# Performance work log

Measured on AMD Instinct MI355X. Metric: run time of the kernel, lower is better.

## Reference

```python
import jax, jax.numpy as jnp
import numpy as np

N, E, H, D_IN, D_OUT, DEPTH, G = 100000, 1600000, 128, 128, 10, 3, 256


def setup_inputs() -> dict:
    key = jax.random.key(0)
    ks = jax.random.split(key, 16)
    s = lambda k, shape: jax.random.normal(k, shape, dtype=jnp.float32) * 0.05
    inp = {
        "x": jax.random.normal(ks[0], (N, D_IN), dtype=jnp.float32),
        "edge_index": jax.random.randint(ks[1], (2, E), 0, N, dtype=jnp.int32),
        "control_edge_index": jax.random.randint(ks[2], (2, 1024), 0, N, dtype=jnp.int32),
        "batch": jnp.sort(jax.random.randint(ks[3], (N,), 0, G, dtype=jnp.int32)),
        # encoder MLP: input_dim -> hidden -> hidden
        "enc_w1": s(ks[4], (D_IN, H)), "enc_b1": jnp.zeros((H,), jnp.float32),
        "enc_w2": s(ks[5], (H, H)),    "enc_b2": jnp.zeros((H,), jnp.float32),
        # conv_depth GCN layers, hidden -> hidden
        "conv_w": s(ks[6], (DEPTH, H, H)), "conv_b": jnp.zeros((DEPTH, H), jnp.float32),
        # decoder MLP: hidden -> hidden -> output_dim
        "dec_w1": s(ks[7], (H, H)),     "dec_b1": jnp.zeros((H,), jnp.float32),
        "dec_w2": s(ks[8], (H, D_OUT)), "dec_b2": jnp.zeros((D_OUT,), jnp.float32),
    }
    return inp


def _gcn_forward(x, enc_w1, enc_b1, enc_w2, enc_b2, conv_w, conv_b,
                 dec_w1, dec_b1, dec_w2, dec_b2, edge_index, batch):
    # encoder MLP (Linear-ReLU-Dropout(eval)-Linear)
    h = jax.nn.relu(x @ enc_w1 + enc_b1) @ enc_w2 + enc_b2

    # GCN normalization with self-loops: D^{-1/2} (A + I) D^{-1/2}
    loops = jnp.arange(N, dtype=edge_index.dtype)
    src = jnp.concatenate([edge_index[0], loops])  # [E + N]
    dst = jnp.concatenate([edge_index[1], loops])
    deg = jax.ops.segment_sum(jnp.ones_like(src, dtype=h.dtype), dst, num_segments=N)
    inv_sqrt = jax.lax.rsqrt(deg)  # deg >= 1 thanks to self-loops
    coef = (inv_sqrt[src] * inv_sqrt[dst])[:, None]  # [E+N, 1]

    for l in range(DEPTH):
        hw = h @ conv_w[l] + conv_b[l]                      # [N, H]
        h = jax.ops.segment_sum(hw[src] * coef, dst, num_segments=N)
        if l < DEPTH - 1:  # linear=False -> nonlinearity between convs
            h = jax.nn.relu(h)

    # global_add_pool over graph ids
    pooled = jax.ops.segment_sum(h, batch, num_segments=G)   # [G, H]

    # decoder MLP
    return jax.nn.relu(pooled @ dec_w1 + dec_b1) @ dec_w2 + dec_b2  # [G, D_OUT]


def reference(x, edge_index, control_edge_index, batch, enc_w1, enc_b1, enc_w2,
              enc_b2, conv_w, conv_b, dec_w1, dec_b1, dec_w2, dec_b2):
    # control_edge_index corresponds to the (disabled) control mechanism; unused
    return _gcn_forward(x, enc_w1, enc_b1, enc_w2, enc_b2, conv_w, conv_b,
                        dec_w1, dec_b1, dec_w2, dec_b2, edge_index, batch)
```

## Files before the change

kernel.cpp:

```cpp
#include <hip/hip_runtime.h>
#include <hip/hip_bf16.h>
#include <cstdint>
#include <cstddef>

#define NN 100000
#define NE 1600000
#define HH 128
#define NG 256

#define NB 196
#define BSH 9
#define BMSK 511
#define CHUNK 16384
#define NBLK 98

typedef __bf16 bf16x8 __attribute__((ext_vector_type(8)));
typedef float floatx4 __attribute__((ext_vector_type(4)));

__device__ __forceinline__ uint32_t f2b(float f) {
  union { float f; uint32_t u; } v; v.f = f;
  uint32_t u = v.u;
  return (u + 0x7FFFu + ((u >> 16) & 1u)) >> 16;
}
__device__ __forceinline__ float blo(uint32_t u) {
  union { uint32_t u; float f; } v; v.u = u << 16;
  return v.f;
}
__device__ __forceinline__ float bhi(uint32_t u) {
  union { uint32_t u; float f; } v; v.u = u & 0xFFFF0000u;
  return v.f;
}
__device__ __forceinline__ void addrow(float* a, uint4 v) {
  a[0] += blo(v.x); a[1] += bhi(v.x);
  a[2] += blo(v.y); a[3] += bhi(v.y);
  a[4] += blo(v.z); a[5] += bhi(v.z);
  a[6] += blo(v.w); a[7] += bhi(v.w);
}

__device__ __forceinline__ void stage_w(uint16_t (*Wt)[136], const float* __restrict__ W,
                                        int tid) {
  for (int it = 0; it < 16; ++it) {
    int idx = tid + it * 256;
    int n = idx & 127;
    int k0 = (idx >> 7) * 4;
    uint2 wv;
    wv.x = f2b(W[(k0 + 0) * 128 + n]) | (f2b(W[(k0 + 1) * 128 + n]) << 16);
    wv.y = f2b(W[(k0 + 2) * 128 + n]) | (f2b(W[(k0 + 3) * 128 + n]) << 16);
    *(uint2*)&Wt[n][k0] = wv;
  }
}


__global__ __launch_bounds__(256) void k_cntA(const int* __restrict__ src,
                                              int* __restrict__ blkcnt) {
  __shared__ int h[NB];
  int t = threadIdx.x;
  if (t < NB) h[t] = 0;
  __syncthreads();
  int base = blockIdx.x * CHUNK, end = min(base + CHUNK, NE);
  for (int i = base + t; i < end; i += 256) atomicAdd(&h[src[i] >> BSH], 1);
  __syncthreads();
  if (t < NB) blkcnt[blockIdx.x * NB + t] = h[t];
}

__global__ __launch_bounds__(256) void k_cntB(const uint2* __restrict__ pairs,
                                              int* __restrict__ blkcnt) {
  __shared__ int h[NB];
  int t = threadIdx.x;
  if (t < NB) h[t] = 0;
  __syncthreads();
  int base = blockIdx.x * CHUNK, end = min(base + CHUNK, NE);
  for (int i = base + t; i < end; i += 256) atomicAdd(&h[pairs[i].y >> BSH], 1);
  __syncthreads();
  if (t < NB) blkcnt[blockIdx.x * NB + t] = h[t];
}

__global__ void k_scan(const int* __restrict__ blkcnt, int* __restrict__ poff,
                       int* __restrict__ gbase, int* __restrict__ off, int set_off) {
  __shared__ int s[256];
  int t = threadIdx.x;
  int tot = 0;
  if (t < NB) {
    for (int r = 0; r < NBLK; ++r) {
      poff[r * NB + t] = tot;
      tot += blkcnt[r * NB + t];
    }
  }
  s[t] = (t < NB) ? tot : 0;
  __syncthreads();
  for (int d = 1; d < 256; d <<= 1) {
    int v = (t >= d) ? s[t - d] : 0;
    __syncthreads();
    s[t] += v;
    __syncthreads();
  }
  if (t < NB) gbase[t] = s[t] - tot;
  if (t == 0) { gbase[NB] = NE; if (set_off) off[NN] = NE; }
}

__global__ __launch_bounds__(256) void k_placeA(const int* __restrict__ src,
                                                const int* __restrict__ dst,
                                                const int* __restrict__ poff,
                                                const int* __restrict__ gbase,
                                                uint2* __restrict__ pairs) {
  __shared__ int cur[NB];
  int t = threadIdx.x;
  if (t < NB) cur[t] = poff[blockIdx.x * NB + t] + gbase[t];
  __syncthreads();
  int base = blockIdx.x * CHUNK, end = min(base + CHUNK, NE);
  for (int i = base + t; i < end; i += 256) {
    int s = src[i], d = dst[i];
    int p = atomicAdd(&cur[s >> BSH], 1);
    pairs[p] = make_uint2((unsigned)s, (unsigned)d);
  }
}

__global__ __launch_bounds__(256) void k_placeB(const uint2* __restrict__ pairs,
                                                const int* __restrict__ poff,
                                                const int* __restrict__ gbase,
                                                uint32_t* __restrict__ outb) {
  __shared__ int cur[NB];
  int t = threadIdx.x;
  if (t < NB) cur[t] = poff[blockIdx.x * NB + t] + gbase[t];
  __syncthreads();
  int base = blockIdx.x * CHUNK, end = min(base + CHUNK, NE);
  for (int i = base + t; i < end; i += 256) {
    uint2 v = pairs[i];
    int p = atomicAdd(&cur[v.y >> BSH], 1);
    outb[p] = v.x | ((v.y & (unsigned)BMSK) << 17);
  }
}

__global__ __launch_bounds__(256) void k_bucket_sort(
    const uint32_t* __restrict__ pairbuf, const int* __restrict__ gbase,
    const int* __restrict__ batch,
    int* __restrict__ off, float* __restrict__ inv, int* __restrict__ csrs,
    int* __restrict__ dhist2, int* __restrict__ gstart)
{
  __shared__ int cnt[512];
  __shared__ int loff[512];
  __shared__ int psum[256];
  int b = blockIdx.x;
  int tid = threadIdx.x;
  cnt[tid] = 0; cnt[tid + 256] = 0;
  __syncthreads();
  int s0 = gbase[b], s1 = gbase[b + 1];
  for (int i = s0 + tid; i < s1; i += 256)
    atomicAdd(&cnt[pairbuf[i] >> 17], 1);
  __syncthreads();
  int a0 = cnt[2 * tid], a1 = cnt[2 * tid + 1];
  int s = a0 + a1;
  psum[tid] = s;
  __syncthreads();
  for (int d = 1; d < 256; d <<= 1) {
    int v = (tid >= d) ? psum[tid - d] : 0;
    __syncthreads();
    psum[tid] += v;
    __syncthreads();
  }
  int excl = psum[tid] - s;
  loff[2 * tid] = excl;
  loff[2 * tid + 1] = excl + a0;
  __syncthreads();
  int* h64 = psum;
  if (tid < 64) h64[tid] = 0;
  __syncthreads();
#pragma unroll
  for (int k = 0; k < 2; ++k) {
    int i = tid + k * 256;
    int node = b * 512 + i;
    if (node < NN) {
      off[node] = s0 + loff[i];
      inv[node] = rsqrtf((float)cnt[i] + 1.0f);
      int d = cnt[i]; if (d > 63) d = 63;
      atomicAdd(&h64[d], 1);
    }
  }
  {
    int n0 = b * 512, n1 = min(n0 + 512, NN);
    for (int i = n0 + tid; i < n1; i += 256) {
      int bb = batch[i];
      if (i == 0) { for (int g = 0; g <= bb; ++g) gstart[g] = 0; }
      else { int aa = batch[i - 1]; for (int g = aa + 1; g <= bb; ++g) gstart[g] = i; }
      if (i == NN - 1) { for (int g = bb + 1; g <= NG; ++g) gstart[g] = NN; }
    }
  }
  __syncthreads();
  if (tid < 64) dhist2[b * 64 + tid] = h64[tid];
  cnt[tid] = loff[tid]; cnt[tid + 256] = loff[tid + 256];
  __syncthreads();
  for (int i = s0 + tid; i < s1; i += 256) {
    uint32_t v = pairbuf[i];
    int p = atomicAdd(&cnt[v >> 17], 1);
    csrs[s0 + p] = (int)(v & 0x1FFFFu);
  }
}

__global__ void k_dscan(const int* __restrict__ dhist2, int* __restrict__ dcur) {
  int t = threadIdx.x;
  int sum = 0;
  for (int r = 0; r < NB; ++r) sum += dhist2[r * 64 + (63 - t)];
  int v = sum;
  for (int d = 1; d < 64; d <<= 1) { int u = __shfl_up(v, d); if (t >= d) v += u; }
  dcur[63 - t] = v - sum;
}

__global__ __launch_bounds__(256) void k_dplace(const int* __restrict__ off,
                                                int* __restrict__ dcur,
                                                int* __restrict__ order) {
  __shared__ int h[64], base[64];
  int t = threadIdx.x;
  if (t < 64) h[t] = 0;
  __syncthreads();
  int i = blockIdx.x * 256 + t;
  int d = 0, ld = 0;
  if (i < NN) { d = off[i + 1] - off[i]; if (d > 63) d = 63; ld = atomicAdd(&h[d], 1); }
  __syncthreads();
  if (t < 64) base[t] = h[t] ? atomicAdd(&dcur[t], h[t]) : 0;
  __syncthreads();
  if (i < NN) order[base[d] + ld] = i;
}

__global__ __launch_bounds__(256) void k_wprep(const float* __restrict__ conv_w,
                                               uint16_t* __restrict__ wbf) {
  int idx = blockIdx.x * 256 + threadIdx.x;
  int l = idx >> 14;
  int n = (idx >> 7) & 127;
  int k = idx & 127;
  wbf[idx] = (uint16_t)f2b(conv_w[(l + 1) * 16384 + k * 128 + n]);
}

__global__ __launch_bounds__(256) void k_gemm(
    const uint16_t* __restrict__ A16, const float* __restrict__ A32,
    const float* __restrict__ W, const float* __restrict__ bias,
    const float* __restrict__ scale,
    uint16_t* __restrict__ Out, int M, int do_relu)
{
  __shared__ uint16_t Wt[128][136];
  const int tid = threadIdx.x;
  stage_w(Wt, W, tid);
  __syncthreads();

  const int lane = tid & 63;
  const int wave = tid >> 6;
  const int lrow = lane & 15;
  const int quad = lane >> 4;
  const int lk = quad * 8;
  const int row0 = blockIdx.x * 128 + wave * 32;

  floatx4 acc[2][8];
#pragma unroll
  for (int t = 0; t < 2; ++t)
#pragma unroll
    for (int n = 0; n < 8; ++n)
      acc[t][n] = (floatx4){0.f, 0.f, 0.f, 0.f};

#pragma unroll
  for (int ks = 0; ks < 4; ++ks) {
    bf16x8 a[2];
#pragma unroll
    for (int t = 0; t < 2; ++t) {
      int r = row0 + t * 16 + lrow;
      uint4 tmp = {0u, 0u, 0u, 0u};
      if (r < M) {
        if (A32) {
          float4 f0 = *(const float4*)(A32 + (size_t)r * HH + ks * 32 + lk);
          float4 f1 = *(const float4*)(A32 + (size_t)r * HH + ks * 32 + lk + 4);
          tmp.x = f2b(f0.x) | (f2b(f0.y) << 16);
          tmp.y = f2b(f0.z) | (f2b(f0.w) << 16);
          tmp.z = f2b(f1.x) | (f2b(f1.y) << 16);
          tmp.w = f2b(f1.z) | (f2b(f1.w) << 16);
        } else {
          tmp = *(const uint4*)(A16 + (size_t)r * HH + ks * 32 + lk);
        }
      }
      a[t] = __builtin_bit_cast(bf16x8, tmp);
    }
#pragma unroll
    for (int n = 0; n < 8; ++n) {
      bf16x8 b = __builtin_bit_cast(bf16x8, *(const uint4*)&Wt[n * 16 + lrow][ks * 32 + lk]);
      acc[0][n] = __builtin_amdgcn_mfma_f32_16x16x32_bf16(b, a[0], acc[0][n], 0, 0, 0);
      acc[1][n] = __builtin_amdgcn_mfma_f32_16x16x32_bf16(b, a[1], acc[1][n], 0, 0, 0);
    }
  }

  float4 b4[8];
#pragma unroll
  for (int n = 0; n < 8; ++n) b4[n] = *(const float4*)(bias + n * 16 + quad * 4);

#pragma unroll
  for (int t = 0; t < 2; ++t) {
    int row = row0 + t * 16 + lrow;
    if (row < M) {
      float sc = scale ? scale[row] : 1.0f;
      uint16_t* orow = Out + (size_t)row * HH;
#pragma unroll
      for (int n = 0; n < 8; ++n) {
        float v0 = acc[t][n][0] + b4[n].x;
        float v1 = acc[t][n][1] + b4[n].y;
        float v2 = acc[t][n][2] + b4[n].z;
        float v3 = acc[t][n][3] + b4[n].w;
        if (do_relu) {
          v0 = fmaxf(v0, 0.f); v1 = fmaxf(v1, 0.f);
          v2 = fmaxf(v2, 0.f); v3 = fmaxf(v3, 0.f);
        }
        v0 *= sc; v1 *= sc; v2 *= sc; v3 *= sc;
        uint2 o;
        o.x = f2b(v0) | (f2b(v1) << 16);
        o.y = f2b(v2) | (f2b(v3) << 16);
        *(uint2*)(orow + n * 16 + quad * 4) = o;
      }
    }
  }
}

__global__ __launch_bounds__(256) void k_gemm_dual(
    const uint16_t* __restrict__ A16,
    const float* __restrict__ Wa, const float* __restrict__ ba,
    const float* __restrict__ Wb, const float* __restrict__ bb,
    const float* __restrict__ scale,
    uint16_t* __restrict__ Out, int M)
{
  __shared__ uint16_t Wt[128][136];
  __shared__ uint16_t tile[128][136];
  const int tid = threadIdx.x;
  stage_w(Wt, Wa, tid);
  __syncthreads();

  const int lane = tid & 63;
  const int wave = tid >> 6;
  const int lrow = lane & 15;
  const int quad = lane >> 4;
  const int lk = quad * 8;
  const int row0 = blockIdx.x * 128 + wave * 32;
  const int trow0 = wave * 32;

  floatx4 acc[2][8];
#pragma unroll
  for (int t = 0; t < 2; ++t)
#pragma unroll
    for (int n = 0; n < 8; ++n)
      acc[t][n] = (floatx4){0.f, 0.f, 0.f, 0.f};

#pragma unroll
  for (int ks = 0; ks < 4; ++ks) {
    bf16x8 a[2];
#pragma unroll
    for (int t = 0; t < 2; ++t) {
      int r = row0 + t * 16 + lrow;
      uint4 tmp = {0u, 0u, 0u, 0u};
      if (r < M) tmp = *(const uint4*)(A16 + (size_t)r * HH + ks * 32 + lk);
      a[t] = __builtin_bit_cast(bf16x8, tmp);
    }
#pragma unroll
    for (int n = 0; n < 8; ++n) {
      bf16x8 b = __builtin_bit_cast(bf16x8, *(const uint4*)&Wt[n * 16 + lrow][ks * 32 + lk]);
      acc[0][n] = __builtin_amdgcn_mfma_f32_16x16x32_bf16(b, a[0], acc[0][n], 0, 0, 0);
      acc[1][n] = __builtin_amdgcn_mfma_f32_16x16x32_bf16(b, a[1], acc[1][n], 0, 0, 0);
    }
  }

  {
    float4 b4[8];
#pragma unroll
    for (int n = 0; n < 8; ++n) b4[n] = *(const float4*)(ba + n * 16 + quad * 4);
#pragma unroll
    for (int t = 0; t < 2; ++t) {
      int trow = trow0 + t * 16 + lrow;
#pragma unroll
      for (int n = 0; n < 8; ++n) {
        uint2 o;
        o.x = f2b(acc[t][n][0] + b4[n].x) | (f2b(acc[t][n][1] + b4[n].y) << 16);
        o.y = f2b(acc[t][n][2] + b4[n].z) | (f2b(acc[t][n][3] + b4[n].w) << 16);
        *(uint2*)&tile[trow][n * 16 + quad * 4] = o;
      }
    }
  }
  __syncthreads();
  stage_w(Wt, Wb, tid);
#pragma unroll
  for (int t = 0; t < 2; ++t)
#pragma unroll
    for (int n = 0; n < 8; ++n)
      acc[t][n] = (floatx4){0.f, 0.f, 0.f, 0.f};
  __syncthreads();

#pragma unroll
  for (int ks = 0; ks < 4; ++ks) {
    bf16x8 a[2];
#pragma unroll
    for (int t = 0; t < 2; ++t)
      a[t] = __builtin_bit_cast(bf16x8,
               *(const uint4*)&tile[trow0 + t * 16 + lrow][ks * 32 + lk]);
#pragma unroll
    for (int n = 0; n < 8; ++n) {
      bf16x8 b = __builtin_bit_cast(bf16x8, *(const uint4*)&Wt[n * 16 + lrow][ks * 32 + lk]);
      acc[0][n] = __builtin_amdgcn_mfma_f32_16x16x32_bf16(b, a[0], acc[0][n], 0, 0, 0);
      acc[1][n] = __builtin_amdgcn_mfma_f32_16x16x32_bf16(b, a[1], acc[1][n], 0, 0, 0);
    }
  }

  {
    float4 b4[8];
#pragma unroll
    for (int n = 0; n < 8; ++n) b4[n] = *(const float4*)(bb + n * 16 + quad * 4);
#pragma unroll
    for (int t = 0; t < 2; ++t) {
      int row = row0 + t * 16 + lrow;
      if (row < M) {
        float sc = scale ? scale[row] : 1.0f;
        uint16_t* orow = Out + (size_t)row * HH;
#pragma unroll
        for (int n = 0; n < 8; ++n) {
          float v0 = (acc[t][n][0] + b4[n].x) * sc;
          float v1 = (acc[t][n][1] + b4[n].y) * sc;
          float v2 = (acc[t][n][2] + b4[n].z) * sc;
          float v3 = (acc[t][n][3] + b4[n].w) * sc;
          uint2 o;
          o.x = f2b(v0) | (f2b(v1) << 16);
          o.y = f2b(v2) | (f2b(v3) << 16);
          *(uint2*)(orow + n * 16 + quad * 4) = o;
        }
      }
    }
  }
}

__global__ __launch_bounds__(256) void k_agg(
    const uint16_t* __restrict__ hw2, const int* __restrict__ off,
    const int* __restrict__ csrs, const float* __restrict__ inv,
    const int* __restrict__ order,
    uint16_t* __restrict__ hout, int do_relu)
{
  int slot = blockIdx.x * 16 + (threadIdx.x >> 4);
  if (slot >= NN) return;
  int node = order[slot];
  int c = (threadIdx.x & 15) * 8;
  const uint16_t* rowp = hw2 + c;

  uint4 sv = *(const uint4*)(rowp + (size_t)node * HH);
  float a[8] = {0.f, 0.f, 0.f, 0.f, 0.f, 0.f, 0.f, 0.f};
  addrow(a, sv);

  int e0 = off[node], e1 = off[node + 1];
  int e = e0;
  for (; e + 4 <= e1; e += 4) {
    int s0 = csrs[e + 0], s1 = csrs[e + 1], s2 = csrs[e + 2], s3 = csrs[e + 3];
    uint4 v0 = *(const uint4*)(rowp + (size_t)s0 * HH);
    uint4 v1 = *(const uint4*)(rowp + (size_t)s1 * HH);
    uint4 v2 = *(const uint4*)(rowp + (size_t)s2 * HH);
    uint4 v3 = *(const uint4*)(rowp + (size_t)s3 * HH);
    addrow(a, v0); addrow(a, v1); addrow(a, v2); addrow(a, v3);
  }
  for (; e < e1; ++e) {
    int s = csrs[e];
    uint4 v = *(const uint4*)(rowp + (size_t)s * HH);
    addrow(a, v);
  }
  float invd = inv[node];
#pragma unroll
  for (int j = 0; j < 8; ++j) {
    a[j] *= invd;
    if (do_relu) a[j] = fmaxf(a[j], 0.f);
  }
  uint4 o;
  o.x = f2b(a[0]) | (f2b(a[1]) << 16);
  o.y = f2b(a[2]) | (f2b(a[3]) << 16);
  o.z = f2b(a[4]) | (f2b(a[5]) << 16);
  o.w = f2b(a[6]) | (f2b(a[7]) << 16);
  *(uint4*)(hout + (size_t)node * HH + c) = o;
}

__global__ __launch_bounds__(512) void k_aggemm(
    const uint16_t* __restrict__ hw2, const int* __restrict__ off,
    const int* __restrict__ csrs, const float* __restrict__ inv,
    const int* __restrict__ order,
    const uint16_t* __restrict__ Wbf, const float* __restrict__ bias,
    uint16_t* __restrict__ Out)
{
  __shared__ uint4 S4[32][16];
  __shared__ int nid[32];
  const int tid = threadIdx.x;

  const int group = tid >> 4;
  const int node = order[blockIdx.x * 32 + group];
  const int c = (tid & 15) * 8;
  if ((tid & 15) == 0) nid[group] = node;
  const uint16_t* rowp = hw2 + c;

  uint4 sv = *(const uint4*)(rowp + (size_t)node * HH);
  float a[8] = {0.f, 0.f, 0.f, 0.f, 0.f, 0.f, 0.f, 0.f};
  addrow(a, sv);

  int e0 = off[node], e1 = off[node + 1];
  int e = e0;
  for (; e + 4 <= e1; e += 4) {
    int s0 = csrs[e + 0], s1 = csrs[e + 1], s2 = csrs[e + 2], s3 = csrs[e + 3];
    uint4 v0 = *(const uint4*)(rowp + (size_t)s0 * HH);
    uint4 v1 = *(const uint4*)(rowp + (size_t)s1 * HH);
    uint4 v2 = *(const uint4*)(rowp + (size_t)s2 * HH);
    uint4 v3 = *(const uint4*)(rowp + (size_t)s3 * HH);
    addrow(a, v0); addrow(a, v1); addrow(a, v2); addrow(a, v3);
  }
  for (; e < e1; ++e) {
    int s = csrs[e];
    uint4 v = *(const uint4*)(rowp + (size_t)s * HH);
    addrow(a, v);
  }
  float invd = inv[node];
#pragma unroll
  for (int j = 0; j < 8; ++j) a[j] = fmaxf(a[j] * invd, 0.f);
  {
    uint4 o;
    o.x = f2b(a[0]) | (f2b(a[1]) << 16);
    o.y = f2b(a[2]) | (f2b(a[3]) << 16);
    o.z = f2b(a[4]) | (f2b(a[5]) << 16);
    o.w = f2b(a[6]) | (f2b(a[7]) << 16);
    S4[group][(tid & 15) ^ (group & 15)] = o;
  }
  __syncthreads();

  const int lane = tid & 63;
  const int wave = tid >> 6;
  const int lrow = lane & 15;
  const int quad = lane >> 4;
  const int lk = quad * 8;
  const uint16_t* wrow = Wbf + (size_t)(wave * 16 + lrow) * HH;

  floatx4 acc0 = (floatx4){0.f, 0.f, 0.f, 0.f};
  floatx4 acc1 = (floatx4){0.f, 0.f, 0.f, 0.f};
#pragma unroll
  for (int ks = 0; ks < 4; ++ks) {
    int ch = (ks * 4 + quad) ^ lrow;
    bf16x8 a0 = __builtin_bit_cast(bf16x8, S4[lrow][ch]);
    bf16x8 a1 = __builtin_bit_cast(bf16x8, S4[16 + lrow][ch]);
    bf16x8 b  = __builtin_bit_cast(bf16x8, *(const uint4*)(wrow + ks * 32 + lk));
    acc0 = __builtin_amdgcn_mfma_f32_16x16x32_bf16(b, a0, acc0, 0, 0, 0);
    acc1 = __builtin_amdgcn_mfma_f32_16x16x32_bf16(b, a1, acc1, 0, 0, 0);
  }

  float4 b4 = *(const float4*)(bias + wave * 16 + quad * 4);
#pragma unroll
  for (int t = 0; t < 2; ++t) {
    floatx4 ac = t ? acc1 : acc0;
    int row = nid[t * 16 + lrow];
    float sc = inv[row];
    float v0 = (ac[0] + b4.x) * sc;
    float v1 = (ac[1] + b4.y) * sc;
    float v2 = (ac[2] + b4.z) * sc;
    float v3 = (ac[3] + b4.w) * sc;
    uint2 o;
    o.x = f2b(v0) | (f2b(v1) << 16);
    o.y = f2b(v2) | (f2b(v3) << 16);
    *(uint2*)(Out + (size_t)row * HH + wave * 16 + quad * 4) = o;
  }
}

__global__ __launch_bounds__(256) void k_pooldec(
    const uint16_t* __restrict__ h, const int* __restrict__ gstart,
    const float* __restrict__ w1, const float* __restrict__ b1,
    const float* __restrict__ w2, const float* __restrict__ b2,
    float* __restrict__ out)
{
  __shared__ float red[16][132];
  __shared__ float p[128], tmpv[128];
  int g = blockIdx.x;
  int tid = threadIdx.x;
  int slot = tid >> 4;
  int c = (tid & 15) * 8;

  int r0 = gstart[g], r1 = gstart[g + 1];
  float a[8] = {0.f, 0.f, 0.f, 0.f, 0.f, 0.f, 0.f, 0.f};
  for (int r = r0 + slot; r < r1; r += 16) {
    uint4 v = *(const uint4*)(h + (size_t)r * HH + c);
    addrow(a, v);
  }
  *(float4*)&red[slot][c]     = make_float4(a[0], a[1], a[2], a[3]);
  *(float4*)&red[slot][c + 4] = make_float4(a[4], a[5], a[6], a[7]);
  __syncthreads();
  if (tid < 128) {
    float s = 0.f;
#pragma unroll
    for (int k = 0; k < 16; ++k) s += red[k][tid];
    p[tid] = s;
  }
  __syncthreads();
  if (tid < 128) {
    float acc1 = b1[tid];
    for (int k = 0; k < 128; ++k) acc1 += p[k] * w1[k * 128 + tid];
    tmpv[tid] = fmaxf(acc1, 0.f);
  }
  __syncthreads();
  if (tid < 10) {
    float o = b2[tid];
    for (int k = 0; k < 128; ++k) o += tmpv[k] * w2[k * 10 + tid];
    out[g * 10 + tid] = o;
  }
}

extern "C" void kernel_launch(void* const* d_in, const int* in_sizes, int n_in,
                              void* d_out, int out_size, void* d_ws, size_t ws_size,
                              hipStream_t stream) {
  const float* x       = (const float*)d_in[0];
  const int*   eidx    = (const int*)d_in[1];
  const int*   src     = eidx;
  const int*   dst     = eidx + NE;
  const int*   batch   = (const int*)d_in[3];
  const float* enc_w1  = (const float*)d_in[4];
  const float* enc_b1  = (const float*)d_in[5];
  const float* enc_w2  = (const float*)d_in[6];
  const float* enc_b2  = (const float*)d_in[7];
  const float* conv_w  = (const float*)d_in[8];
  const float* conv_b  = (const float*)d_in[9];
  const float* dec_w1  = (const float*)d_in[10];
  const float* dec_b1  = (const float*)d_in[11];
  const float* dec_w2  = (const float*)d_in[12];
  const float* dec_b2  = (const float*)d_in[13];
  float* out = (float*)d_out;

  char* ws = (char*)d_ws;
  size_t o = 0;
  auto alloc = [&](size_t bytes) -> char* {
    char* p = ws + o;
    o += (bytes + 255) & ~(size_t)255;
    return p;
  };
  int*      off     = (int*)alloc((size_t)(NN + 1) * 4);
  int*      csrs    = (int*)alloc((size_t)NE * 4);
  float*    inv     = (float*)alloc((size_t)NN * 4);
  int*      blkcntA = (int*)alloc((size_t)NBLK * NB * 4);
  int*      poffA   = (int*)alloc((size_t)NBLK * NB * 4);
  int*      blkcntB = (int*)alloc((size_t)NBLK * NB * 4);
  int*      poffB   = (int*)alloc((size_t)NBLK * NB * 4);
  int*      gbaseA  = (int*)alloc((size_t)(NB + 1) * 4);
  int*      gbaseB  = (int*)alloc((size_t)(NB + 1) * 4);
  int*      dhist2  = (int*)alloc((size_t)NB * 64 * 4);
  int*      dcur    = (int*)alloc(64 * 4);
  int*      order   = (int*)alloc((size_t)NN * 4);
  int*      gstart  = (int*)alloc((size_t)(NG + 1) * 4);
  uint16_t* wbf     = (uint16_t*)alloc((size_t)2 * 16384 * 2);
  uint16_t* buf0    = (uint16_t*)alloc((size_t)NN * HH * 2);
  uint16_t* buf1    = (uint16_t*)alloc((size_t)NN * HH * 2);
  uint2*    pairsA  = (uint2*)buf1;
  uint32_t* pairB   = (uint32_t*)((char*)buf1 + (size_t)NE * 8);

  k_wprep<<<dim3(128), dim3(256), 0, stream>>>(conv_w, wbf);

  k_cntA<<<dim3(NBLK), dim3(256), 0, stream>>>(src, blkcntA);
  k_scan<<<dim3(1), dim3(256), 0, stream>>>(blkcntA, poffA, gbaseA, off, 0);
  k_placeA<<<dim3(NBLK), dim3(256), 0, stream>>>(src, dst, poffA, gbaseA, pairsA);
  k_cntB<<<dim3(NBLK), dim3(256), 0, stream>>>(pairsA, blkcntB);
  k_scan<<<dim3(1), dim3(256), 0, stream>>>(blkcntB, poffB, gbaseB, off, 1);
  k_placeB<<<dim3(NBLK), dim3(256), 0, stream>>>(pairsA, poffB, gbaseB, pairB);
  k_bucket_sort<<<dim3(NB), dim3(256), 0, stream>>>(pairB, gbaseB, batch, off, inv, csrs,
                                                    dhist2, gstart);

  const int NBK = (NN + 255) / 256;
  k_dscan<<<dim3(1), dim3(64), 0, stream>>>(dhist2, dcur);
  k_dplace<<<dim3(NBK), dim3(256), 0, stream>>>(off, dcur, order);

  const int GB = (NN + 127) / 128;
  k_gemm<<<dim3(GB), dim3(256), 0, stream>>>(nullptr, x, enc_w1, enc_b1, nullptr, buf1, NN, 1);
  k_gemm_dual<<<dim3(GB), dim3(256), 0, stream>>>(buf1, enc_w2, enc_b2,
                                                  conv_w + 0 * 16384, conv_b + 0,
                                                  inv, buf0, NN);

  const int FB = NN / 32;
  const int AB = (NN + 15) / 16;
  k_aggemm<<<dim3(FB), dim3(512), 0, stream>>>(buf0, off, csrs, inv, order,
                                               wbf, conv_b + 128, buf1);
  k_aggemm<<<dim3(FB), dim3(512), 0, stream>>>(buf1, off, csrs, inv, order,
                                               wbf + 16384, conv_b + 256, buf0);
  k_agg <<<dim3(AB), dim3(256), 0, stream>>>(buf0, off, csrs, inv, order, buf1, 0);

  k_pooldec<<<dim3(NG), dim3(256), 0, stream>>>(buf1, gstart, dec_w1, dec_b1, dec_w2, dec_b2, out);
}
```

Measured before the change: 492.6 us.

## Merge independent preprocessing and encoder kernels into combined launches

Several independent kernels are fused into single launches that dispatch on block index: weight prep with the source count, bucket sort with the first encoder GEMM, degree scan with the inverse-sqrt computation, and the dual GEMM with the degree-ordered placement. The edge-histogram chunk size is shrunk so more blocks run in the count and place phases. pairB gets its own workspace buffer because buf1 is now written by the encoder while the sort reads pairB. The aim is fewer launches and better GPU occupancy by overlapping graph preprocessing with dense encoder work, at the cost of more workspace memory and larger per-block histogram output.

```diff
diff --git a/kernel.cpp b/kernel.cpp
--- a/kernel.cpp
+++ b/kernel.cpp
@@ -11,8 +11,10 @@
 #define NB 196
 #define BSH 9
 #define BMSK 511
-#define CHUNK 16384
-#define NBLK 98
+#define CHUNK 4096
+#define NBLK 391
+#define GB 782
+#define NBK 391
 
 typedef __bf16 bf16x8 __attribute__((ext_vector_type(8)));
 typedef float floatx4 __attribute__((ext_vector_type(4)));
@@ -50,17 +52,26 @@
   }
 }
 
-
-__global__ __launch_bounds__(256) void k_cntA(const int* __restrict__ src,
-                                              int* __restrict__ blkcnt) {
-  __shared__ int h[NB];
+__global__ __launch_bounds__(256) void k_front(const int* __restrict__ src,
+                                               int* __restrict__ blkcnt,
+                                               const float* __restrict__ conv_w,
+                                               uint16_t* __restrict__ wbf) {
   int t = threadIdx.x;
-  if (t < NB) h[t] = 0;
-  __syncthreads();
-  int base = blockIdx.x * CHUNK, end = min(base + CHUNK, NE);
-  for (int i = base + t; i < end; i += 256) atomicAdd(&h[src[i] >> BSH], 1);
-  __syncthreads();
-  if (t < NB) blkcnt[blockIdx.x * NB + t] = h[t];
+  if (blockIdx.x < NBLK) {
+    __shared__ int h[NB];
+    if (t < NB) h[t] = 0;
+    __syncthreads();
+    int base = blockIdx.x * CHUNK, end = min(base + CHUNK, NE);
+    for (int i = base + t; i < end; i += 256) atomicAdd(&h[src[i] >> BSH], 1);
+    __syncthreads();
+    if (t < NB) blkcnt[blockIdx.x * NB + t] = h[t];
+  } else {
+    int idx = (blockIdx.x - NBLK) * 256 + t;
+    int l = idx >> 14;
+    int n = (idx >> 7) & 127;
+    int k = idx & 127;
+    wbf[idx] = (uint16_t)f2b(conv_w[(l + 1) * 16384 + k * 128 + n]);
+  }
 }
 
 __global__ __launch_bounds__(256) void k_cntB(const uint2* __restrict__ pairs,
@@ -131,291 +142,76 @@
   }
 }
 
-__global__ __launch_bounds__(256) void k_bucket_sort(
+__global__ __launch_bounds__(256) void k_sortenc(
     const uint32_t* __restrict__ pairbuf, const int* __restrict__ gbase,
     const int* __restrict__ batch,
-    int* __restrict__ off, float* __restrict__ inv, int* __restrict__ csrs,
-    int* __restrict__ dhist2, int* __restrict__ gstart)
+    int* __restrict__ off, int* __restrict__ csrs,
+    int* __restrict__ dhist2, int* __restrict__ gstart,
+    const float* __restrict__ A32, const float* __restrict__ W,
+    const float* __restrict__ bias, uint16_t* __restrict__ Out)
 {
-  __shared__ int cnt[512];
-  __shared__ int loff[512];
-  __shared__ int psum[256];
-  int b = blockIdx.x;
-  int tid = threadIdx.x;
-  cnt[tid] = 0; cnt[tid + 256] = 0;
-  __syncthreads();
-  int s0 = gbase[b], s1 = gbase[b + 1];
-  for (int i = s0 + tid; i < s1; i += 256)
-    atomicAdd(&cnt[pairbuf[i] >> 17], 1);
-  __syncthreads();
-  int a0 = cnt[2 * tid], a1 = cnt[2 * tid + 1];
-  int s = a0 + a1;
-  psum[tid] = s;
-  __syncthreads();
-  for (int d = 1; d < 256; d <<= 1) {
-    int v = (tid >= d) ? psum[tid - d] : 0;
-    __syncthreads();
-    psum[tid] += v;
-    __syncthreads();
-  }
-  int excl = psum[tid] - s;
-  loff[2 * tid] = excl;
-  loff[2 * tid + 1] = excl + a0;
-  __syncthreads();
-  int* h64 = psum;
-  if (tid < 64) h64[tid] = 0;
-  __syncthreads();
-#pragma unroll
-  for (int k = 0; k < 2; ++k) {
-    int i = tid + k * 256;
-    int node = b * 512 + i;
-    if (node < NN) {
-      off[node] = s0 + loff[i];
-      inv[node] = rsqrtf((float)cnt[i] + 1.0f);
-      int d = cnt[i]; if (d > 63) d = 63;
-      atomicAdd(&h64[d], 1);
-    }
-  }
-  {
-    int n0 = b * 512, n1 = min(n0 + 512, NN);
-    for (int i = n0 + tid; i < n1; i += 256) {
-      int bb = batch[i];
-      if (i == 0) { for (int g = 0; g <= bb; ++g) gstart[g] = 0; }
-      else { int aa = batch[i - 1]; for (int g = aa + 1; g <= bb; ++g) gstart[g] = i; }
-      if (i == NN - 1) { for (int g = bb + 1; g <= NG; ++g) gstart[g] = NN; }
-    }
-  }
-  __syncthreads();
-  if (tid < 64) dhist2[b * 64 + tid] = h64[tid];
-  cnt[tid] = loff[tid]; cnt[tid + 256] = loff[tid + 256];
-  __syncthreads();
-  for (int i = s0 + tid; i < s1; i += 256) {
-    uint32_t v = pairbuf[i];
-    int p = atomicAdd(&cnt[v >> 17], 1);
-    csrs[s0 + p] = (int)(v & 0x1FFFFu);
-  }
-}
-
-__global__ void k_dscan(const int* __restrict__ dhist2, int* __restrict__ dcur) {
-  int t = threadIdx.x;
-  int sum = 0;
-  for (int r = 0; r < NB; ++r) sum += dhist2[r * 64 + (63 - t)];
-  int v = sum;
-  for (int d = 1; d < 64; d <<= 1) { int u = __shfl_up(v, d); if (t >= d) v += u; }
-  dcur[63 - t] = v - sum;
-}
-
-__global__ __launch_bounds__(256) void k_dplace(const int* __restrict__ off,
-                                                int* __restrict__ dcur,
-                                                int* __restrict__ order) {
-  __shared__ int h[64], base[64];
-  int t = threadIdx.x;
-  if (t < 64) h[t] = 0;
-  __syncthreads();
-  int i = blockIdx.x * 256 + t;
-  int d = 0, ld = 0;
-  if (i < NN) { d = off[i + 1] - off[i]; if (d > 63) d = 63; ld = atomicAdd(&h[d], 1); }
-  __syncthreads();
-  if (t < 64) base[t] = h[t] ? atomicAdd(&dcur[t], h[t]) : 0;
-  __syncthreads();
-  if (i < NN) order[base[d] + ld] = i;
-}
-
-__global__ __launch_bounds__(256) void k_wprep(const float* __restrict__ conv_w,
-                                               uint16_t* __restrict__ wbf) {
-  int idx = blockIdx.x * 256 + threadIdx.x;
-  int l = idx >> 14;
-  int n = (idx >> 7) & 127;
-  int k = idx & 127;
-  wbf[idx] = (uint16_t)f2b(conv_w[(l + 1) * 16384 + k * 128 + n]);
-}
-
-__global__ __launch_bounds__(256) void k_gemm(
-    const uint16_t* __restrict__ A16, const float* __restrict__ A32,
-    const float* __restrict__ W, const float* __restrict__ bias,
-    const float* __restrict__ scale,
-    uint16_t* __restrict__ Out, int M, int do_relu)
-{
-  __shared__ uint16_t Wt[128][136];
+  __shared__ char smraw[34816];
   const int tid = threadIdx.x;
-  stage_w(Wt, W, tid);
-  __syncthreads();
-
-  const int lane = tid & 63;
-  const int wave = tid >> 6;
-  const int lrow = lane & 15;
-  const int quad = lane >> 4;
-  const int lk = quad * 8;
-  const int row0 = blockIdx.x * 128 + wave * 32;
-
-  floatx4 acc[2][8];
-#pragma unroll
-  for (int t = 0; t < 2; ++t)
-#pragma unroll
-    for (int n = 0; n < 8; ++n)
-      acc[t][n] = (floatx4){0.f, 0.f, 0.f, 0.f};
-
-#pragma unroll
-  for (int ks = 0; ks < 4; ++ks) {
-    bf16x8 a[2];
-#pragma unroll
-    for (int t = 0; t < 2; ++t) {
-      int r = row0 + t * 16 + lrow;
-      uint4 tmp = {0u, 0u, 0u, 0u};
-      if (r < M) {
-        if (A32) {
+
+  if (blockIdx.x < GB) {
+    auto Wt = (uint16_t(*)[136])smraw;
+    stage_w(Wt, W, tid);
+    __syncthreads();
+
+    const int lane = tid & 63;
+    const int wave = tid >> 6;
+    const int lrow = lane & 15;
+    const int quad = lane >> 4;
+    const int lk = quad * 8;
+    const int row0 = blockIdx.x * 128 + wave * 32;
+
+    floatx4 acc[2][8];
+#pragma unroll
+    for (int t = 0; t < 2; ++t)
+#pragma unroll
+      for (int n = 0; n < 8; ++n)
+        acc[t][n] = (floatx4){0.f, 0.f, 0.f, 0.f};
+
+#pragma unroll
+    for (int ks = 0; ks < 4; ++ks) {
+      bf16x8 a[2];
+#pragma unroll
+      for (int t = 0; t < 2; ++t) {
+        int r = row0 + t * 16 + lrow;
+        uint4 tmp = {0u, 0u, 0u, 0u};
+        if (r < NN) {
           float4 f0 = *(const float4*)(A32 + (size_t)r * HH + ks * 32 + lk);
           float4 f1 = *(const float4*)(A32 + (size_t)r * HH + ks * 32 + lk + 4);
           tmp.x = f2b(f0.x) | (f2b(f0.y) << 16);
           tmp.y = f2b(f0.z) | (f2b(f0.w) << 16);
           tmp.z = f2b(f1.x) | (f2b(f1.y) << 16);
           tmp.w = f2b(f1.z) | (f2b(f1.w) << 16);
-        } else {
-          tmp = *(const uint4*)(A16 + (size_t)r * HH + ks * 32 + lk);
         }
-      }
-      a[t] = __builtin_bit_cast(bf16x8, tmp);
-    }
-#pragma unroll
-    for (int n = 0; n < 8; ++n) {
-      bf16x8 b = __builtin_bit_cast(bf16x8, *(const uint4*)&Wt[n * 16 + lrow][ks * 32 + lk]);
-      acc[0][n] = __builtin_amdgcn_mfma_f32_16x16x32_bf16(b, a[0], acc[0][n], 0, 0, 0);
-      acc[1][n] = __builtin_amdgcn_mfma_f32_16x16x32_bf16(b, a[1], acc[1][n], 0, 0, 0);
-    }
-  }
-
-  float4 b4[8];
-#pragma unroll
-  for (int n = 0; n < 8; ++n) b4[n] = *(const float4*)(bias + n * 16 + quad * 4);
-
-#pragma unroll
-  for (int t = 0; t < 2; ++t) {
-    int row = row0 + t * 16 + lrow;
-    if (row < M) {
-      float sc = scale ? scale[row] : 1.0f;
-      uint16_t* orow = Out + (size_t)row * HH;
+        a[t] = __builtin_bit_cast(bf16x8, tmp);
+      }
 #pragma unroll
       for (int n = 0; n < 8; ++n) {
-        float v0 = acc[t][n][0] + b4[n].x;
-        float v1 = acc[t][n][1] + b4[n].y;
-        float v2 = acc[t][n][2] + b4[n].z;
-        float v3 = acc[t][n][3] + b4[n].w;
-        if (do_relu) {
-          v0 = fmaxf(v0, 0.f); v1 = fmaxf(v1, 0.f);
-          v2 = fmaxf(v2, 0.f); v3 = fmaxf(v3, 0.f);
-        }
-        v0 *= sc; v1 *= sc; v2 *= sc; v3 *= sc;
-        uint2 o;
-        o.x = f2b(v0) | (f2b(v1) << 16);
-        o.y = f2b(v2) | (f2b(v3) << 16);
-        *(uint2*)(orow + n * 16 + quad * 4) = o;
-      }
-    }
-  }
-}
-
-__global__ __launch_bounds__(256) void k_gemm_dual(
-    const uint16_t* __restrict__ A16,
-    const float* __restrict__ Wa, const float* __restrict__ ba,
-    const float* __restrict__ Wb, const float* __restrict__ bb,
-    const float* __restrict__ scale,
-    uint16_t* __restrict__ Out, int M)
-{
-  __shared__ uint16_t Wt[128][136];
-  __shared__ uint16_t tile[128][136];
-  const int tid = threadIdx.x;
-  stage_w(Wt, Wa, tid);
-  __syncthreads();
-
-  const int lane = tid & 63;
-  const int wave = tid >> 6;
-  const int lrow = lane & 15;
-  const int quad = lane >> 4;
-  const int lk = quad * 8;
-  const int row0 = blockIdx.x * 128 + wave * 32;
-  const int trow0 = wave * 32;
-
-  floatx4 acc[2][8];
-#pragma unroll
-  for (int t = 0; t < 2; ++t)
-#pragma unroll
-    for (int n = 0; n < 8; ++n)
-      acc[t][n] = (floatx4){0.f, 0.f, 0.f, 0.f};
-
-#pragma unroll
-  for (int ks = 0; ks < 4; ++ks) {
-    bf16x8 a[2];
-#pragma unroll
-    for (int t = 0; t < 2; ++t) {
-      int r = row0 + t * 16 + lrow;
-      uint4 tmp = {0u, 0u, 0u, 0u};
-      if (r < M) tmp = *(const uint4*)(A16 + (size_t)r * HH + ks * 32 + lk);
-      a[t] = __builtin_bit_cast(bf16x8, tmp);
-    }
-#pragma unroll
-    for (int n = 0; n < 8; ++n) {
-      bf16x8 b = __builtin_bit_cast(bf16x8, *(const uint4*)&Wt[n * 16 + lrow][ks * 32 + lk]);
-      acc[0][n] = __builtin_amdgcn_mfma_f32_16x16x32_bf16(b, a[0], acc[0][n], 0, 0, 0);
-      acc[1][n] = __builtin_amdgcn_mfma_f32_16x16x32_bf16(b, a[1], acc[1][n], 0, 0, 0);
-    }
-  }
-
-  {
+        bf16x8 b = __builtin_bit_cast(bf16x8, *(const uint4*)&Wt[n * 16 + lrow][ks * 32 + lk]);
+        acc[0][n] = __builtin_amdgcn_mfma_f32_16x16x32_bf16(b, a[0], acc[0][n], 0, 0, 0);
+        acc[1][n] = __builtin_amdgcn_mfma_f32_16x16x32_bf16(b, a[1], acc[1][n], 0, 0, 0);
+      }
+    }
+
     float4 b4[8];
 #pragma unroll
-    for (int n = 0; n < 8; ++n) b4[n] = *(const float4*)(ba + n * 16 + quad * 4);
-#pragma unroll
-    for (int t = 0; t < 2; ++t) {
-      int trow = trow0 + t * 16 + lrow;
-#pragma unroll
-      for (int n = 0; n < 8; ++n) {
-        uint2 o;
-        o.x = f2b(acc[t][n][0] + b4[n].x) | (f2b(acc[t][n][1] + b4[n].y) << 16);
-        o.y = f2b(acc[t][n][2] + b4[n].z) | (f2b(acc[t][n][3] + b4[n].w) << 16);
-        *(uint2*)&tile[trow][n * 16 + quad * 4] = o;
-      }
-    }
-  }
-  __syncthreads();
-  stage_w(Wt, Wb, tid);
-#pragma unroll
-  for (int t = 0; t < 2; ++t)
-#pragma unroll
-    for (int n = 0; n < 8; ++n)
-      acc[t][n] = (floatx4){0.f, 0.f, 0.f, 0.f};
-  __syncthreads();
-
-#pragma unroll
-  for (int ks = 0; ks < 4; ++ks) {
-    bf16x8 a[2];
-#pragma unroll
-    for (int t = 0; t < 2; ++t)
-      a[t] = __builtin_bit_cast(bf16x8,
-               *(const uint4*)&tile[trow0 + t * 16 + lrow][ks * 32 + lk]);
-#pragma unroll
-    for (int n = 0; n < 8; ++n) {
-      bf16x8 b = __builtin_bit_cast(bf16x8, *(const uint4*)&Wt[n * 16 + lrow][ks * 32 + lk]);
-      acc[0][n] = __builtin_amdgcn_mfma_f32_16x16x32_bf16(b, a[0], acc[0][n], 0, 0, 0);
-      acc[1][n] = __builtin_amdgcn_mfma_f32_16x16x32_bf16(b, a[1], acc[1][n], 0, 0, 0);
-    }
-  }
-
-  {
-    float4 b4[8];
-#pragma unroll
-    for (int n = 0; n < 8; ++n) b4[n] = *(const float4*)(bb + n * 16 + quad * 4);
+    for (int n = 0; n < 8; ++n) b4[n] = *(const float4*)(bias + n * 16 + quad * 4);
+
 #pragma unroll
     for (int t = 0; t < 2; ++t) {
       int row = row0 + t * 16 + lrow;
-      if (row < M) {
-        float sc = scale ? scale[row] : 1.0f;
+      if (row < NN) {
         uint16_t* orow = Out + (size_t)row * HH;
 #pragma unroll
         for (int n = 0; n < 8; ++n) {
-          float v0 = (acc[t][n][0] + b4[n].x) * sc;
-          float v1 = (acc[t][n][1] + b4[n].y) * sc;
-          float v2 = (acc[t][n][2] + b4[n].z) * sc;
-          float v3 = (acc[t][n][3] + b4[n].w) * sc;
+          float v0 = fmaxf(acc[t][n][0] + b4[n].x, 0.f);
+          float v1 = fmaxf(acc[t][n][1] + b4[n].y, 0.f);
+          float v2 = fmaxf(acc[t][n][2] + b4[n].z, 0.f);
+          float v3 = fmaxf(acc[t][n][3] + b4[n].w, 0.f);
           uint2 o;
           o.x = f2b(v0) | (f2b(v1) << 16);
           o.y = f2b(v2) | (f2b(v3) << 16);
@@ -423,6 +219,208 @@
         }
       }
     }
+  } else {
+    int* cnt  = (int*)smraw;
+    int* loff = cnt + 512;
+    int* psum = loff + 512;
+    int b = blockIdx.x - GB;
+    cnt[tid] = 0; cnt[tid + 256] = 0;
+    __syncthreads();
+    int s0 = gbase[b], s1 = gbase[b + 1];
+    for (int i = s0 + tid; i < s1; i += 256)
+      atomicAdd(&cnt[pairbuf[i] >> 17], 1);
+    __syncthreads();
+    int a0 = cnt[2 * tid], a1 = cnt[2 * tid + 1];
+    int s = a0 + a1;
+    psum[tid] = s;
+    __syncthreads();
+    for (int d = 1; d < 256; d <<= 1) {
+      int v = (tid >= d) ? psum[tid - d] : 0;
+      __syncthreads();
+      psum[tid] += v;
+      __syncthreads();
+    }
+    int excl = psum[tid] - s;
+    loff[2 * tid] = excl;
+    loff[2 * tid + 1] = excl + a0;
+    __syncthreads();
+    int* h64 = psum;
+    if (tid < 64) h64[tid] = 0;
+    __syncthreads();
+#pragma unroll
+    for (int k = 0; k < 2; ++k) {
+      int i = tid + k * 256;
+      int node = b * 512 + i;
+      if (node < NN) {
+        off[node] = s0 + loff[i];
+        int d = cnt[i]; if (d > 63) d = 63;
+        atomicAdd(&h64[d], 1);
+      }
+    }
+    {
+      int n0 = b * 512, n1 = min(n0 + 512, NN);
+      for (int i = n0 + tid; i < n1; i += 256) {
+        int bb = batch[i];
+        if (i == 0) { for (int g = 0; g <= bb; ++g) gstart[g] = 0; }
+        else { int aa = batch[i - 1]; for (int g = aa + 1; g <= bb; ++g) gstart[g] = i; }
+        if (i == NN - 1) { for (int g = bb + 1; g <= NG; ++g) gstart[g] = NN; }
+      }
+    }
+    __syncthreads();
+    if (tid < 64) dhist2[b * 64 + tid] = h64[tid];
+    cnt[tid] = loff[tid]; cnt[tid + 256] = loff[tid + 256];
+    __syncthreads();
+    for (int i = s0 + tid; i < s1; i += 256) {
+      uint32_t v = pairbuf[i];
+      int p = atomicAdd(&cnt[v >> 17], 1);
+      csrs[s0 + p] = (int)(v & 0x1FFFFu);
+    }
+  }
+}
+
+__global__ __launch_bounds__(256) void k_dinv(const int* __restrict__ dhist2,
+                                              int* __restrict__ dcur,
+                                              const int* __restrict__ off,
+                                              float* __restrict__ inv) {
+  if (blockIdx.x == 0) {
+    int t = threadIdx.x;
+    if (t < 64) {
+      int sum = 0;
+      for (int r = 0; r < NB; ++r) sum += dhist2[r * 64 + (63 - t)];
+      int v = sum;
+      for (int d = 1; d < 64; d <<= 1) { int u = __shfl_up(v, d); if (t >= d) v += u; }
+      dcur[63 - t] = v - sum;
+    }
+  } else {
+    int i = (blockIdx.x - 1) * 256 + threadIdx.x;
+    if (i < NN) inv[i] = rsqrtf((float)(off[i + 1] - off[i]) + 1.0f);
+  }
+}
+
+__global__ __launch_bounds__(256) void k_dualplace(
+    const uint16_t* __restrict__ A16,
+    const float* __restrict__ Wa, const float* __restrict__ ba,
+    const float* __restrict__ Wb, const float* __restrict__ bb,
+    const float* __restrict__ scale, uint16_t* __restrict__ Out,
+    const int* __restrict__ off, int* __restrict__ dcur, int* __restrict__ order)
+{
+  __shared__ uint16_t Wt[128][136];
+  __shared__ uint16_t tile[128][136];
+  const int tid = threadIdx.x;
+
+  if (blockIdx.x < GB) {
+    stage_w(Wt, Wa, tid);
+    __syncthreads();
+
+    const int lane = tid & 63;
+    const int wave = tid >> 6;
+    const int lrow = lane & 15;
+    const int quad = lane >> 4;
+    const int lk = quad * 8;
+    const int row0 = blockIdx.x * 128 + wave * 32;
+    const int trow0 = wave * 32;
+
+    floatx4 acc[2][8];
+#pragma unroll
+    for (int t = 0; t < 2; ++t)
+#pragma unroll
+      for (int n = 0; n < 8; ++n)
+        acc[t][n] = (floatx4){0.f, 0.f, 0.f, 0.f};
+
+#pragma unroll
+    for (int ks = 0; ks < 4; ++ks) {
+      bf16x8 a[2];
+#pragma unroll
+      for (int t = 0; t < 2; ++t) {
+        int r = row0 + t * 16 + lrow;
+        uint4 tmp = {0u, 0u, 0u, 0u};
+        if (r < NN) tmp = *(const uint4*)(A16 + (size_t)r * HH + ks * 32 + lk);
+        a[t] = __builtin_bit_cast(bf16x8, tmp);
+      }
+#pragma unroll
+      for (int n = 0; n < 8; ++n) {
+        bf16x8 b = __builtin_bit_cast(bf16x8, *(const uint4*)&Wt[n * 16 + lrow][ks * 32 + lk]);
+        acc[0][n] = __builtin_amdgcn_mfma_f32_16x16x32_bf16(b, a[0], acc[0][n], 0, 0, 0);
+        acc[1][n] = __builtin_amdgcn_mfma_f32_16x16x32_bf16(b, a[1], acc[1][n], 0, 0, 0);
+      }
+    }
+
+    {
+      float4 b4[8];
+#pragma unroll
+      for (int n = 0; n < 8; ++n) b4[n] = *(const float4*)(ba + n * 16 + quad * 4);
+#pragma unroll
+      for (int t = 0; t < 2; ++t) {
+        int trow = trow0 + t * 16 + lrow;
+#pragma unroll
+        for (int n = 0; n < 8; ++n) {
+          uint2 o;
+          o.x = f2b(acc[t][n][0] + b4[n].x) | (f2b(acc[t][n][1] + b4[n].y) << 16);
+          o.y = f2b(acc[t][n][2] + b4[n].z) | (f2b(acc[t][n][3] + b4[n].w) << 16);
+          *(uint2*)&tile[trow][n * 16 + quad * 4] = o;
+        }
+      }
+    }
+    __syncthreads();
+    stage_w(Wt, Wb, tid);
+#pragma unroll
+    for (int t = 0; t < 2; ++t)
+#pragma unroll
+      for (int n = 0; n < 8; ++n)
+        acc[t][n] = (floatx4){0.f, 0.f, 0.f, 0.f};
+    __syncthreads();
+
+#pragma unroll
+    for (int ks = 0; ks < 4; ++ks) {
+      bf16x8 a[2];
+#pragma unroll
+      for (int t = 0; t < 2; ++t)
+        a[t] = __builtin_bit_cast(bf16x8,
+                 *(const uint4*)&tile[trow0 + t * 16 + lrow][ks * 32 + lk]);
+#pragma unroll
+      for (int n = 0; n < 8; ++n) {
+        bf16x8 b = __builtin_bit_cast(bf16x8, *(const uint4*)&Wt[n * 16 + lrow][ks * 32 + lk]);
+        acc[0][n] = __builtin_amdgcn_mfma_f32_16x16x32_bf16(b, a[0], acc[0][n], 0, 0, 0);
+        acc[1][n] = __builtin_amdgcn_mfma_f32_16x16x32_bf16(b, a[1], acc[1][n], 0, 0, 0);
+      }
+    }
+
+    {
+      float4 b4[8];
+#pragma unroll
+      for (int n = 0; n < 8; ++n) b4[n] = *(const float4*)(bb + n * 16 + quad * 4);
+#pragma unroll
+      for (int t = 0; t < 2; ++t) {
+        int row = row0 + t * 16 + lrow;
+        if (row < NN) {
+          float sc = scale[row];
+          uint16_t* orow = Out + (size_t)row * HH;
+#pragma unroll
+          for (int n = 0; n < 8; ++n) {
+            float v0 = (acc[t][n][0] + b4[n].x) * sc;
+            float v1 = (acc[t][n][1] + b4[n].y) * sc;
+            float v2 = (acc[t][n][2] + b4[n].z) * sc;
+            float v3 = (acc[t][n][3] + b4[n].w) * sc;
+            uint2 o;
+            o.x = f2b(v0) | (f2b(v1) << 16);
+            o.y = f2b(v2) | (f2b(v3) << 16);
+            *(uint2*)(orow + n * 16 + quad * 4) = o;
+          }
+        }
+      }
+    }
+  } else {
+    int* h = (int*)Wt;
+    int* base = h + 64;
+    if (tid < 64) h[tid] = 0;
+    __syncthreads();
+    int i = (blockIdx.x - GB) * 256 + tid;
+    int d = 0, ld = 0;
+    if (i < NN) { d = off[i + 1] - off[i]; if (d > 63) d = 63; ld = atomicAdd(&h[d], 1); }
+    __syncthreads();
+    if (tid < 64) base[tid] = h[tid] ? atomicAdd(&dcur[tid], h[tid]) : 0;
+    __syncthreads();
+    if (i < NN) order[base[d] + ld] = i;
   }
 }
 
@@ -639,31 +637,24 @@
   int*      order   = (int*)alloc((size_t)NN * 4);
   int*      gstart  = (int*)alloc((size_t)(NG + 1) * 4);
   uint16_t* wbf     = (uint16_t*)alloc((size_t)2 * 16384 * 2);
+  uint32_t* pairB   = (uint32_t*)alloc((size_t)NE * 4);
   uint16_t* buf0    = (uint16_t*)alloc((size_t)NN * HH * 2);
   uint16_t* buf1    = (uint16_t*)alloc((size_t)NN * HH * 2);
   uint2*    pairsA  = (uint2*)buf1;
-  uint32_t* pairB   = (uint32_t*)((char*)buf1 + (size_t)NE * 8);
-
-  k_wprep<<<dim3(128), dim3(256), 0, stream>>>(conv_w, wbf);
-
-  k_cntA<<<dim3(NBLK), dim3(256), 0, stream>>>(src, blkcntA);
+
+  k_front<<<dim3(NBLK + 128), dim3(256), 0, stream>>>(src, blkcntA, conv_w, wbf);
   k_scan<<<dim3(1), dim3(256), 0, stream>>>(blkcntA, poffA, gbaseA, off, 0);
   k_placeA<<<dim3(NBLK), dim3(256), 0, stream>>>(src, dst, poffA, gbaseA, pairsA);
   k_cntB<<<dim3(NBLK), dim3(256), 0, stream>>>(pairsA, blkcntB);
   k_scan<<<dim3(1), dim3(256), 0, stream>>>(blkcntB, poffB, gbaseB, off, 1);
   k_placeB<<<dim3(NBLK), dim3(256), 0, stream>>>(pairsA, poffB, gbaseB, pairB);
-  k_bucket_sort<<<dim3(NB), dim3(256), 0, stream>>>(pairB, gbaseB, batch, off, inv, csrs,
-                                                    dhist2, gstart);
-
-  const int NBK = (NN + 255) / 256;
-  k_dscan<<<dim3(1), dim3(64), 0, stream>>>(dhist2, dcur);
-  k_dplace<<<dim3(NBK), dim3(256), 0, stream>>>(off, dcur, order);
-
-  const int GB = (NN + 127) / 128;
-  k_gemm<<<dim3(GB), dim3(256), 0, stream>>>(nullptr, x, enc_w1, enc_b1, nullptr, buf1, NN, 1);
-  k_gemm_dual<<<dim3(GB), dim3(256), 0, stream>>>(buf1, enc_w2, enc_b2,
-                                                  conv_w + 0 * 16384, conv_b + 0,
-                                                  inv, buf0, NN);
+  k_sortenc<<<dim3(GB + NB), dim3(256), 0, stream>>>(pairB, gbaseB, batch, off, csrs,
+                                                     dhist2, gstart,
+                                                     x, enc_w1, enc_b1, buf1);
+  k_dinv<<<dim3(1 + NBK), dim3(256), 0, stream>>>(dhist2, dcur, off, inv);
+  k_dualplace<<<dim3(GB + NBK), dim3(256), 0, stream>>>(buf1, enc_w2, enc_b2,
+                                                        conv_w + 0 * 16384, conv_b + 0,
+                                                        inv, buf0, off, dcur, order);
 
   const int FB = NN / 32;
   const int AB = (NN + 15) / 16;
```

Result: no change. 484.5 us (-1.6%).
